# Kernel tuning notes

Measured on AMD Instinct MI355X. Metric: run time of the kernel, lower is better.

Reference implementation:

```python
import jax, jax.numpy as jnp
import numpy as np

L, B, T = 4, 64, 512
H, IN = 1024, 1024


def setup_inputs() -> dict:
    key = jax.random.key(0)
    ks = jax.random.split(key, 6)
    stdv = 1.0 / np.sqrt(H)
    x = jax.random.normal(ks[0], (T, B, IN), dtype=jnp.float32)
    h0 = jax.random.normal(ks[1], (L, B, H), dtype=jnp.float32)
    # stacked per-layer params (input_size == hidden_size so shapes stack)
    w_ih = jax.random.uniform(ks[2], (L, 3 * H, IN), minval=-stdv, maxval=stdv, dtype=jnp.float32)
    w_hh = jax.random.uniform(ks[3], (L, 3 * H, H), minval=-stdv, maxval=stdv, dtype=jnp.float32)
    b_ih = jax.random.uniform(ks[4], (L, 3 * H), minval=-stdv, maxval=stdv, dtype=jnp.float32)
    b_hh = jax.random.uniform(ks[5], (L, 3 * H), minval=-stdv, maxval=stdv, dtype=jnp.float32)
    return {"x": x, "h0": h0, "w_ih": w_ih, "w_hh": w_hh, "b_ih": b_ih, "b_hh": b_hh}


def _gru_forward(x, h0, w_ih, w_hh, b_ih, b_hh):
    hidden = w_hh.shape[-1]

    def layer_fn(inp, layer_args):
        wi, wh, bi, bh, h_prev = layer_args
        gi = inp @ wi.T + bi          # [B, 3H]
        gh = h_prev @ wh.T + bh       # [B, 3H]
        gi_r, gi_z, gi_n = jnp.split(gi, 3, axis=1)
        gh_r, gh_z, gh_n = jnp.split(gh, 3, axis=1)
        r = jax.nn.sigmoid(gi_r + gh_r)
        z = jax.nn.sigmoid(gi_z + gh_z)
        n = jnp.tanh(gi_n + r * gh_n)
        h_new = (1.0 - z) * n + z * h_prev
        return h_new, h_new

    def time_step(h_all, x_t):
        # scan over layers: input flows through, hidden states updated
        _, h_stack = jax.lax.scan(layer_fn, x_t, (w_ih, w_hh, b_ih, b_hh, h_all))
        return h_stack, None

    h_final, _ = jax.lax.scan(time_step, h0, x)
    return h_final  # [L, B, H]


def reference(x, h0, w_ih, w_hh, b_ih, b_hh):
    return _gru_forward(x, h0, w_ih, w_hh, b_ih, b_hh)
```

## Files before the change

### kernel.cpp

```cpp
#include <hip/hip_runtime.h>
#include <hip/hip_bf16.h>

#define NL 4
#define NB 64
#define NT 512
#define NH 1024
#define N3H 3072
#define BH 65536
#define HS_SLOTS 513
#define FSTRIDE 4

typedef __attribute__((ext_vector_type(8))) short short8;
typedef __attribute__((ext_vector_type(4))) float floatx4;

__device__ __forceinline__ short8 ld8(const __hip_bfloat16* p) {
  return *(const short8*)p;
}


__global__ void conv_w_kernel(const float* __restrict__ w_ih,
                              const float* __restrict__ w_hh,
                              __hip_bfloat16* __restrict__ wih_b,
                              __hip_bfloat16* __restrict__ whh_hi,
                              __hip_bfloat16* __restrict__ whh_lo_n) {
  size_t i = (size_t)blockIdx.x * 256 + threadIdx.x;
  if (i >= (size_t)NL * N3H * NH) return;
  wih_b[i] = __float2bfloat16(w_ih[i]);
  float v = w_hh[i];
  __hip_bfloat16 hi = __float2bfloat16(v);
  whh_hi[i] = hi;
  size_t l = i / ((size_t)N3H * NH);
  size_t rem = i - l * ((size_t)N3H * NH);
  size_t row = rem / NH;
  if (row >= (size_t)2 * NH) {
    size_t k = rem - row * NH;
    whh_lo_n[(l * NH + (row - 2 * NH)) * NH + k] =
        __float2bfloat16(v - __bfloat162float(hi));
  }
}

__global__ void conv_x_kernel(const float* __restrict__ x,
                              __hip_bfloat16* __restrict__ xb) {
  size_t i = (size_t)blockIdx.x * 256 + threadIdx.x;
  if (i >= (size_t)NT * NB * NH) return;
  xb[i] = __float2bfloat16(x[i]);
}

__global__ void init_wave_kernel(const float* __restrict__ h0,
                                 float* __restrict__ out,
                                 __hip_bfloat16* __restrict__ hseq,
                                 int* __restrict__ flags) {
  size_t i = (size_t)blockIdx.x * 256 + threadIdx.x;
  if (i < (size_t)5 * 64 * FSTRIDE)
    flags[i] = (i < (size_t)4 * 64 * FSTRIDE) ? 0 : 0x3fffffff;
  if (i >= (size_t)NL * NB * NH) return;
  out[i] = h0[i];
  size_t l = i >> 16;
  size_t j = i & (BH - 1);
  hseq[l * (size_t)HS_SLOTS * BH + j] = __float2bfloat16(h0[i]);
}

__global__ __launch_bounds__(256, 1) void gru_wave_kernel(
    const __hip_bfloat16* __restrict__ whh_hi,
    const __hip_bfloat16* __restrict__ whh_lo,
    const __hip_bfloat16* __restrict__ wih,
    const __hip_bfloat16* __restrict__ xb,
    const float* __restrict__ b_ih,
    const float* __restrict__ b_hh,
    __hip_bfloat16* hseq,
    float* __restrict__ out,
    int* flags) {
  extern __shared__ short lds[];
  const int tid = threadIdx.x;
  const int wv = tid >> 6, lane = tid & 63;
  const int l = blockIdx.x >> 6, g = blockIdx.x & 63;
  const int l15 = lane & 15, quad = lane >> 4;
  const int u = g * 16 + l15;

  const size_t l3h = (size_t)l * N3H;

  {
    const __hip_bfloat16* src;
    if (wv == 0)      src = whh_hi + (l3h + 2 * NH + u) * NH + quad * 8;
    else if (wv == 1) src = whh_lo + (((size_t)l * NH) + u) * NH + quad * 8;
    else if (wv == 2) src = whh_hi + (l3h + u) * NH + quad * 8;
    else              src = whh_hi + (l3h + NH + u) * NH + quad * 8;
    short* dst = lds + wv * 16384 + lane * 8;
#pragma unroll 4
    for (int kc = 0; kc < 32; ++kc)
      *(short8*)(dst + kc * 512) = ld8(src + kc * 32);
  }
  __syncthreads();

  const __hip_bfloat16* vr = wih + (l3h + u) * NH + quad * 8;
  const __hip_bfloat16* vz = wih + (l3h + NH + u) * NH + quad * 8;
  const __hip_bfloat16* vn = wih + (l3h + 2 * NH + u) * NH + quad * 8;
  const float bir = b_ih[l3h + u], biz = b_ih[l3h + NH + u],
              bin = b_ih[l3h + 2 * NH + u];
  const float bhr = b_hh[l3h + u], bhz = b_hh[l3h + NH + u],
              bhn = b_hh[l3h + 2 * NH + u];

  __hip_bfloat16* hs_l = hseq + (size_t)l * HS_SLOTS * BH;
  const __hip_bfloat16* upbase =
      l ? hseq + (size_t)(l - 1) * HS_SLOTS * BH : xb;
  const int upoff = l ? 1 : 0;

  const int row0 = wv * 16 + quad * 4;
  const size_t arow = (size_t)(wv * 16 + l15) * NH + quad * 8;

  float hreg[4];
#pragma unroll
  for (int r = 0; r < 4; ++r)
    hreg[r] = out[(size_t)l * BH + (size_t)(row0 + r) * NH + u];

  const int* fo = flags + (l * 64 + lane) * FSTRIDE;
  const int* fu = flags + ((l ? (l - 1) : 4) * 64 + lane) * FSTRIDE;
  int* fmine = flags + (l * 64 + g) * FSTRIDE;

#pragma unroll 1
  for (int t = 0; t < NT; ++t) {
    while (__hip_atomic_load(fo, __ATOMIC_RELAXED, __HIP_MEMORY_SCOPE_AGENT) < t)
      __builtin_amdgcn_s_sleep(1);
    while (__hip_atomic_load(fu, __ATOMIC_RELAXED, __HIP_MEMORY_SCOPE_AGENT) < t + 1)
      __builtin_amdgcn_s_sleep(1);
    __builtin_amdgcn_sched_barrier(0);
    asm volatile("" ::: "memory");

    const __hip_bfloat16* ob = hs_l + (size_t)t * BH + arow;
    const __hip_bfloat16* ub = upbase + (size_t)(t + upoff) * BH + arow;

    floatx4 z4 = {0.f, 0.f, 0.f, 0.f};
    floatx4 ar = z4, az = z4, anh = z4, anl = z4, gr = z4, gz = z4, gn = z4;

#pragma unroll 4
    for (int kc = 0; kc < 32; ++kc) {
      short8 ho = ld8(ob + kc * 32);
      short8 hu = ld8(ub + kc * 32);
      short8 vrf = ld8(vr + kc * 32);
      short8 vzf = ld8(vz + kc * 32);
      short8 vnf = ld8(vn + kc * 32);
      short8 bnh = *(short8*)(lds + lane * 8 + kc * 512);
      short8 bnl = *(short8*)(lds + 16384 + lane * 8 + kc * 512);
      short8 brf = *(short8*)(lds + 32768 + lane * 8 + kc * 512);
      short8 bzf = *(short8*)(lds + 49152 + lane * 8 + kc * 512);
      ar = __builtin_amdgcn_mfma_f32_16x16x32_bf16(ho, brf, ar, 0, 0, 0);
      az = __builtin_amdgcn_mfma_f32_16x16x32_bf16(ho, bzf, az, 0, 0, 0);
      anh = __builtin_amdgcn_mfma_f32_16x16x32_bf16(ho, bnh, anh, 0, 0, 0);
      anl = __builtin_amdgcn_mfma_f32_16x16x32_bf16(ho, bnl, anl, 0, 0, 0);
      gr = __builtin_amdgcn_mfma_f32_16x16x32_bf16(hu, vrf, gr, 0, 0, 0);
      gz = __builtin_amdgcn_mfma_f32_16x16x32_bf16(hu, vzf, gz, 0, 0, 0);
      gn = __builtin_amdgcn_mfma_f32_16x16x32_bf16(hu, vnf, gn, 0, 0, 0);
    }

    __hip_bfloat16* hw = hs_l + (size_t)(t + 1) * BH;
#pragma unroll
    for (int r = 0; r < 4; ++r) {
      float ghr = ar[r] + bhr;
      float ghz = az[r] + bhz;
      float ghn = anh[r] + anl[r] + bhn;
      float gir = gr[r] + bir;
      float giz = gz[r] + biz;
      float gin = gn[r] + bin;
      float rr = 1.f / (1.f + __expf(-(gir + ghr)));
      float zz = 1.f / (1.f + __expf(-(giz + ghz)));
      float xt = gin + rr * ghn;
      xt = fminf(fmaxf(xt, -15.f), 15.f);
      float e2 = __expf(2.f * xt);
      float nn = (e2 - 1.f) / (e2 + 1.f);
      float hn = (1.f - zz) * nn + zz * hreg[r];
      hreg[r] = hn;
      __hip_bfloat16 hb16 = __float2bfloat16(hn);
      unsigned int v32 = (unsigned int)__builtin_bit_cast(unsigned short, hb16);
      asm volatile("global_store_short %0, %1, off sc0 sc1"
                   :: "v"(hw + (size_t)(row0 + r) * NH + u), "v"(v32)
                   : "memory");
    }
    asm volatile("s_waitcnt vmcnt(0)" ::: "memory");
    __syncthreads();
    if (tid == 0)
      __hip_atomic_store(fmine, t + 1, __ATOMIC_RELAXED, __HIP_MEMORY_SCOPE_AGENT);
  }

#pragma unroll
  for (int r = 0; r < 4; ++r)
    out[(size_t)l * BH + (size_t)(row0 + r) * NH + u] = hreg[r];
}


__global__ void init_out_kernel(const float* __restrict__ h0,
                                float* __restrict__ out,
                                int* __restrict__ flags) {
  size_t i = (size_t)blockIdx.x * 256 + threadIdx.x;
  if (i < (size_t)4 * 64 * FSTRIDE) flags[i] = 0;
  if (i >= (size_t)NL * NB * NH) return;
  out[i] = h0[i];
}

__global__ void init_hbf_kernel(const float* __restrict__ h0_layer,
                                __hip_bfloat16* __restrict__ hb) {
  size_t i = (size_t)blockIdx.x * 256 + threadIdx.x;
  if (i >= (size_t)NB * NH) return;
  hb[i] = __float2bfloat16(h0_layer[i]);
}

__global__ __launch_bounds__(256) void gemm_gi_kernel(
    const __hip_bfloat16* __restrict__ A,
    const __hip_bfloat16* __restrict__ Wb,
    const float* __restrict__ bih,
    float* __restrict__ C) {
  __shared__ short lA[128 * 32];
  __shared__ short lB[128 * 32];
  const int tid = threadIdx.x;
  const int wave = tid >> 6, lane = tid & 63;
  const int l15 = lane & 15, quad = lane >> 4;
  const int m0 = blockIdx.x * 128;
  const int n0 = blockIdx.y * 128;
  const int wm = (wave >> 1) * 64, wn = (wave & 1) * 64;

  const int r1 = tid >> 2, c1 = (tid & 3) * 8;
  const __hip_bfloat16* Arow0 = A + (size_t)(m0 + r1) * NH + c1;
  const __hip_bfloat16* Arow1 = A + (size_t)(m0 + r1 + 64) * NH + c1;
  const __hip_bfloat16* Brow0 = Wb + (size_t)(n0 + r1) * NH + c1;
  const __hip_bfloat16* Brow1 = Wb + (size_t)(n0 + r1 + 64) * NH + c1;

  floatx4 z4 = {0.f, 0.f, 0.f, 0.f};
  floatx4 acc[4][4];
#pragma unroll
  for (int mi = 0; mi < 4; ++mi)
#pragma unroll
    for (int ni = 0; ni < 4; ++ni) acc[mi][ni] = z4;

  for (int kt = 0; kt < 32; ++kt) {
    const int ko = kt * 32;
    short8 a0 = ld8(Arow0 + ko), a1 = ld8(Arow1 + ko);
    short8 b0 = ld8(Brow0 + ko), b1 = ld8(Brow1 + ko);
    __syncthreads();
    *(short8*)(lA + tid * 8) = a0;
    *(short8*)(lA + (tid + 256) * 8) = a1;
    *(short8*)(lB + tid * 8) = b0;
    *(short8*)(lB + (tid + 256) * 8) = b1;
    __syncthreads();
    short8 af[4], bf[4];
#pragma unroll
    for (int mi = 0; mi < 4; ++mi)
      af[mi] = *(short8*)(lA + (wm + mi * 16 + l15) * 32 + quad * 8);
#pragma unroll
    for (int ni = 0; ni < 4; ++ni)
      bf[ni] = *(short8*)(lB + (wn + ni * 16 + l15) * 32 + quad * 8);
#pragma unroll
    for (int mi = 0; mi < 4; ++mi)
#pragma unroll
      for (int ni = 0; ni < 4; ++ni)
        acc[mi][ni] =
            __builtin_amdgcn_mfma_f32_16x16x32_bf16(af[mi], bf[ni], acc[mi][ni], 0, 0, 0);
  }

  const int crow = m0 + wm + quad * 4;
#pragma unroll
  for (int ni = 0; ni < 4; ++ni) {
    const int col = n0 + wn + ni * 16 + l15;
    const float bias = bih[col];
#pragma unroll
    for (int mi = 0; mi < 4; ++mi)
#pragma unroll
      for (int r = 0; r < 4; ++r)
        C[(size_t)(crow + mi * 16 + r) * N3H + col] = acc[mi][ni][r] + bias;
  }
}

__global__ __launch_bounds__(64) void gru_persist_kernel(
    const __hip_bfloat16* __restrict__ whh_hi_l,
    const __hip_bfloat16* __restrict__ whh_lo_l,
    const float* __restrict__ gi_c,
    const float* __restrict__ bhh_l,
    __hip_bfloat16* hbuf,
    __hip_bfloat16* seq_out,
    float* hfp,
    int* flags,
    int s0, int nsteps) {
  const int lane = threadIdx.x;
  const int w = blockIdx.x >> 6;
  const int g = blockIdx.x & 63;
  const int l15 = lane & 15, quad = lane >> 4;
  const int u = g * 16 + l15;

  __shared__ short lds_s[32768];

  {
    const __hip_bfloat16* srch = whh_hi_l + ((size_t)(2 * NH) + u) * NH + quad * 8;
    const __hip_bfloat16* srcl = whh_lo_l + (size_t)u * NH + quad * 8;
    short* dst = lds_s + lane * 8;
#pragma unroll 4
    for (int kc = 0; kc < 32; ++kc) {
      *(short8*)(dst + kc * 512) = ld8(srch + kc * 32);
      *(short8*)(dst + 16384 + kc * 512) = ld8(srcl + kc * 32);
    }
  }
  __syncthreads();

  const int bb = w * 16 + quad * 4;
  float hreg[4];
#pragma unroll
  for (int r = 0; r < 4; ++r) hreg[r] = hfp[(size_t)(bb + r) * NH + u];

  const float bhr = bhh_l[u], bhz = bhh_l[NH + u], bhn = bhh_l[2 * NH + u];
  const __hip_bfloat16* wr = whh_hi_l + (size_t)u * NH + quad * 8;
  const __hip_bfloat16* wz = whh_hi_l + ((size_t)NH + u) * NH + quad * 8;

  int* myflag = flags + (w * 64 + lane) * FSTRIDE;
  int* outflag = flags + (w * 64 + g) * FSTRIDE;
  __hip_bfloat16* hb0 = hbuf;
  __hip_bfloat16* hb1 = hbuf + NB * NH;

  for (int s = s0; s < s0 + nsteps; ++s) {
    const int tc = s - s0;
    const float* gp = gi_c + ((size_t)tc * NB + bb) * N3H + u;
    float gi_r[4], gi_z[4], gi_n[4];
#pragma unroll
    for (int r = 0; r < 4; ++r) {
      gi_r[r] = gp[(size_t)r * N3H];
      gi_z[r] = gp[(size_t)r * N3H + NH];
      gi_n[r] = gp[(size_t)r * N3H + 2 * NH];
    }

    while (__hip_atomic_load(myflag, __ATOMIC_RELAXED, __HIP_MEMORY_SCOPE_AGENT) < s)
      __builtin_amdgcn_s_sleep(1);

    const __hip_bfloat16* hbase =
        ((s & 1) ? hb1 : hb0) + (size_t)(w * 16 + l15) * NH + quad * 8;
    short8 hf[32];
#pragma unroll
    for (int kc = 0; kc < 32; ++kc)
      asm volatile("global_load_dwordx4 %0, %1, off sc0 sc1"
                   : "=v"(hf[kc]) : "v"(hbase + kc * 32));
#pragma unroll
    for (int g8 = 0; g8 < 32; g8 += 8)
      asm volatile("s_waitcnt vmcnt(0)"
                   : "+v"(hf[g8]), "+v"(hf[g8 + 1]), "+v"(hf[g8 + 2]),
                     "+v"(hf[g8 + 3]), "+v"(hf[g8 + 4]), "+v"(hf[g8 + 5]),
                     "+v"(hf[g8 + 6]), "+v"(hf[g8 + 7])
                   :: "memory");

    floatx4 accr = {0.f, 0.f, 0.f, 0.f}, accz = accr, accnh = accr, accnl = accr;
#pragma unroll 8
    for (int kc = 0; kc < 32; ++kc) {
      short8 ah = hf[kc];
      short8 brf = ld8(wr + kc * 32);
      short8 bzf = ld8(wz + kc * 32);
      short8 bnh = *(short8*)(lds_s + lane * 8 + kc * 512);
      short8 bnl = *(short8*)(lds_s + 16384 + lane * 8 + kc * 512);
      accr = __builtin_amdgcn_mfma_f32_16x16x32_bf16(ah, brf, accr, 0, 0, 0);
      accz = __builtin_amdgcn_mfma_f32_16x16x32_bf16(ah, bzf, accz, 0, 0, 0);
      accnh = __builtin_amdgcn_mfma_f32_16x16x32_bf16(ah, bnh, accnh, 0, 0, 0);
      accnl = __builtin_amdgcn_mfma_f32_16x16x32_bf16(ah, bnl, accnl, 0, 0, 0);
    }

    __hip_bfloat16* hout = (s & 1) ? hb0 : hb1;
#pragma unroll
    for (int r = 0; r < 4; ++r) {
      float ghr = accr[r] + bhr;
      float ghz = accz[r] + bhz;
      float ghn = accnh[r] + accnl[r] + bhn;
      float rr = 1.f / (1.f + __expf(-(gi_r[r] + ghr)));
      float zz = 1.f / (1.f + __expf(-(gi_z[r] + ghz)));
      float xt = gi_n[r] + rr * ghn;
      xt = fminf(fmaxf(xt, -15.f), 15.f);
      float e2 = __expf(2.f * xt);
      float nn = (e2 - 1.f) / (e2 + 1.f);
      float hn = (1.f - zz) * nn + zz * hreg[r];
      hreg[r] = hn;
      __hip_bfloat16 hb16 = __float2bfloat16(hn);
      size_t idx = (size_t)(bb + r) * NH + u;
      unsigned int v32 = (unsigned int)__builtin_bit_cast(unsigned short, hb16);
      asm volatile("global_store_short %0, %1, off sc0 sc1"
                   :: "v"(hout + idx), "v"(v32) : "memory");
      if (seq_out) seq_out[(size_t)tc * (NB * NH) + idx] = hb16;
    }
    asm volatile("s_waitcnt vmcnt(0)" ::: "memory");
    if (lane == 0)
      __hip_atomic_store(outflag, s + 1, __ATOMIC_RELAXED, __HIP_MEMORY_SCOPE_AGENT);
  }

#pragma unroll
  for (int r = 0; r < 4; ++r) hfp[(size_t)(bb + r) * NH + u] = hreg[r];
}

extern "C" void kernel_launch(void* const* d_in, const int* in_sizes, int n_in,
                              void* d_out, int out_size, void* d_ws, size_t ws_size,
                              hipStream_t stream) {
  const float* x = (const float*)d_in[0];
  const float* h0 = (const float*)d_in[1];
  const float* w_ih = (const float*)d_in[2];
  const float* w_hh = (const float*)d_in[3];
  const float* b_ih = (const float*)d_in[4];
  const float* b_hh = (const float*)d_in[5];
  float* out = (float*)d_out;
  (void)in_sizes; (void)n_in; (void)out_size;

  char* ws = (char*)d_ws;
  const size_t wsz = (size_t)NL * N3H * NH * 2;
  const size_t lsz = (size_t)NL * NH * NH * 2;
  const size_t xsz = (size_t)NT * NB * NH * 2;
  const size_t hssz = (size_t)NL * HS_SLOTS * BH * 2;
  const size_t fsz = (size_t)5 * 64 * FSTRIDE * 4;
  const size_t need_wave = wsz * 2 + lsz + xsz + hssz + fsz + 1024;

  if (ws_size >= need_wave) {
    size_t off = 0;
    __hip_bfloat16* wih_b = (__hip_bfloat16*)(ws + off); off += wsz;
    __hip_bfloat16* whh_hi = (__hip_bfloat16*)(ws + off); off += wsz;
    __hip_bfloat16* whh_lo = (__hip_bfloat16*)(ws + off); off += lsz;
    __hip_bfloat16* xb = (__hip_bfloat16*)(ws + off); off += xsz;
    __hip_bfloat16* hseq = (__hip_bfloat16*)(ws + off); off += hssz;
    int* flags = (int*)(ws + off); off += fsz;

    static bool attr_set = false;
    if (!attr_set) {
      (void)hipFuncSetAttribute((const void*)gru_wave_kernel,
                                hipFuncAttributeMaxDynamicSharedMemorySize,
                                131072);
      attr_set = true;
    }

    {
      size_t n = (size_t)NL * N3H * NH;
      conv_w_kernel<<<dim3((n + 255) / 256), dim3(256), 0, stream>>>(
          w_ih, w_hh, wih_b, whh_hi, whh_lo);
    }
    {
      size_t n = (size_t)NT * NB * NH;
      conv_x_kernel<<<dim3((n + 255) / 256), dim3(256), 0, stream>>>(x, xb);
    }
    {
      size_t n = (size_t)NL * NB * NH;
      init_wave_kernel<<<dim3((n + 255) / 256), dim3(256), 0, stream>>>(
          h0, out, hseq, flags);
    }
    gru_wave_kernel<<<dim3(256), dim3(256), 131072, stream>>>(
        whh_hi, whh_lo, wih_b, xb, b_ih, b_hh, hseq, out, flags);
    return;
  }

  size_t off = 0;
  const size_t ssz = (size_t)NT * NB * NH * 2;
  __hip_bfloat16* wih_b = (__hip_bfloat16*)(ws + off); off += wsz;
  __hip_bfloat16* whh_hi = (__hip_bfloat16*)(ws + off); off += wsz;
  __hip_bfloat16* whh_lo = (__hip_bfloat16*)(ws + off); off += lsz;
  __hip_bfloat16* seqA = (__hip_bfloat16*)(ws + off); off += ssz;
  __hip_bfloat16* seqB = (__hip_bfloat16*)(ws + off); off += ssz;
  __hip_bfloat16* hbuf = (__hip_bfloat16*)(ws + off); off += (size_t)2 * NB * NH * 2;
  int* flags = (int*)(ws + off); off += (size_t)4 * 64 * FSTRIDE * 4;
  off = (off + 255) & ~(size_t)255;
  float* gi_buf = (float*)(ws + off);

  long long avail = (long long)ws_size - (long long)off;
  int TC = 256;
  while (TC > 2 && (long long)TC * NB * N3H * 4 > avail) TC >>= 1;

  {
    size_t n = (size_t)NL * N3H * NH;
    conv_w_kernel<<<dim3((n + 255) / 256), dim3(256), 0, stream>>>(
        w_ih, w_hh, wih_b, whh_hi, whh_lo);
  }
  {
    size_t n = (size_t)NT * NB * NH;
    conv_x_kernel<<<dim3((n + 255) / 256), dim3(256), 0, stream>>>(x, seqA);
  }
  {
    size_t n = (size_t)NL * NB * NH;
    init_out_kernel<<<dim3((n + 255) / 256), dim3(256), 0, stream>>>(h0, out, flags);
  }

  const size_t bh = (size_t)NB * NH;
  const int nchunks = NT / TC;
  for (int l = 0; l < NL; ++l) {
    init_hbf_kernel<<<dim3((bh + 255) / 256), dim3(256), 0, stream>>>(
        h0 + (size_t)l * bh, hbuf);
    const __hip_bfloat16* cur = (l & 1) ? seqB : seqA;
    __hip_bfloat16* nxt = (l == NL - 1) ? (__hip_bfloat16*)nullptr
                                        : ((l & 1) ? seqA : seqB);
    const __hip_bfloat16* wih_l = wih_b + (size_t)l * N3H * NH;
    const __hip_bfloat16* whha_l = whh_hi + (size_t)l * N3H * NH;
    const __hip_bfloat16* whhb_l = whh_lo + (size_t)l * NH * NH;
    const float* bih_l = b_ih + (size_t)l * N3H;
    const float* bhh_l = b_hh + (size_t)l * N3H;
    float* hfp_l = out + (size_t)l * bh;
    for (int c = 0; c < nchunks; ++c) {
      const __hip_bfloat16* Ac = cur + (size_t)c * TC * bh;
      gemm_gi_kernel<<<dim3(TC * NB / 128, N3H / 128), dim3(256), 0, stream>>>(
          Ac, wih_l, bih_l, gi_buf);
      __hip_bfloat16* so = nxt ? nxt + (size_t)c * TC * bh : (__hip_bfloat16*)nullptr;
      gru_persist_kernel<<<dim3(256), dim3(64), 0, stream>>>(
          whha_l, whhb_l, gi_buf, bhh_l, hbuf, so, hfp_l, flags,
          l * NT + c * TC, TC);
    }
  }
}
```

Baseline: 13.11 ms.

## Stage W_in n-gate weights in LDS and prefetch hidden rows into registers

The n-gate input weights are now loaded once into a fifth LDS slab, raising dynamic shared memory to 160KB, so they are no longer streamed from global memory every timestep. The loads of the own-layer and upstream hidden states for all 32 k-chunks are hoisted into register arrays ahead of a fully unrolled MFMA loop, so the loads can be issued together and latency overlapped. The two flag spin-waits are merged into one loop. The larger register arrays raise register pressure and risk spilling, and the larger LDS footprint relies on the MI355X shared memory capacity.

```diff
diff --git a/kernel.cpp b/kernel.cpp
--- a/kernel.cpp
+++ b/kernel.cpp
@@ -89,12 +89,18 @@
 #pragma unroll 4
     for (int kc = 0; kc < 32; ++kc)
       *(short8*)(dst + kc * 512) = ld8(src + kc * 32);
+    const __hip_bfloat16* srcn = wih + (l3h + 2 * NH + u) * NH + quad * 8;
+    short* dstn = lds + 4 * 16384 + lane * 8;
+#pragma unroll
+    for (int kk = 0; kk < 8; ++kk) {
+      int kc = wv * 8 + kk;
+      *(short8*)(dstn + kc * 512) = ld8(srcn + kc * 32);
+    }
   }
   __syncthreads();
 
   const __hip_bfloat16* vr = wih + (l3h + u) * NH + quad * 8;
   const __hip_bfloat16* vz = wih + (l3h + NH + u) * NH + quad * 8;
-  const __hip_bfloat16* vn = wih + (l3h + 2 * NH + u) * NH + quad * 8;
   const float bir = b_ih[l3h + u], biz = b_ih[l3h + NH + u],
               bin = b_ih[l3h + 2 * NH + u];
   const float bhr = b_hh[l3h + u], bhz = b_hh[l3h + NH + u],
@@ -119,9 +125,8 @@
 
 #pragma unroll 1
   for (int t = 0; t < NT; ++t) {
-    while (__hip_atomic_load(fo, __ATOMIC_RELAXED, __HIP_MEMORY_SCOPE_AGENT) < t)
-      __builtin_amdgcn_s_sleep(1);
-    while (__hip_atomic_load(fu, __ATOMIC_RELAXED, __HIP_MEMORY_SCOPE_AGENT) < t + 1)
+    while (__hip_atomic_load(fo, __ATOMIC_RELAXED, __HIP_MEMORY_SCOPE_AGENT) < t ||
+           __hip_atomic_load(fu, __ATOMIC_RELAXED, __HIP_MEMORY_SCOPE_AGENT) < t + 1)
       __builtin_amdgcn_s_sleep(1);
     __builtin_amdgcn_sched_barrier(0);
     asm volatile("" ::: "memory");
@@ -129,27 +134,31 @@
     const __hip_bfloat16* ob = hs_l + (size_t)t * BH + arow;
     const __hip_bfloat16* ub = upbase + (size_t)(t + upoff) * BH + arow;
 
+    short8 ho[32], hu[32];
+#pragma unroll
+    for (int kc = 0; kc < 32; ++kc) ho[kc] = ld8(ob + kc * 32);
+#pragma unroll
+    for (int kc = 0; kc < 32; ++kc) hu[kc] = ld8(ub + kc * 32);
+
     floatx4 z4 = {0.f, 0.f, 0.f, 0.f};
     floatx4 ar = z4, az = z4, anh = z4, anl = z4, gr = z4, gz = z4, gn = z4;
 
-#pragma unroll 4
+#pragma unroll
     for (int kc = 0; kc < 32; ++kc) {
-      short8 ho = ld8(ob + kc * 32);
-      short8 hu = ld8(ub + kc * 32);
       short8 vrf = ld8(vr + kc * 32);
       short8 vzf = ld8(vz + kc * 32);
-      short8 vnf = ld8(vn + kc * 32);
       short8 bnh = *(short8*)(lds + lane * 8 + kc * 512);
       short8 bnl = *(short8*)(lds + 16384 + lane * 8 + kc * 512);
       short8 brf = *(short8*)(lds + 32768 + lane * 8 + kc * 512);
       short8 bzf = *(short8*)(lds + 49152 + lane * 8 + kc * 512);
-      ar = __builtin_amdgcn_mfma_f32_16x16x32_bf16(ho, brf, ar, 0, 0, 0);
-      az = __builtin_amdgcn_mfma_f32_16x16x32_bf16(ho, bzf, az, 0, 0, 0);
-      anh = __builtin_amdgcn_mfma_f32_16x16x32_bf16(ho, bnh, anh, 0, 0, 0);
-      anl = __builtin_amdgcn_mfma_f32_16x16x32_bf16(ho, bnl, anl, 0, 0, 0);
-      gr = __builtin_amdgcn_mfma_f32_16x16x32_bf16(hu, vrf, gr, 0, 0, 0);
-      gz = __builtin_amdgcn_mfma_f32_16x16x32_bf16(hu, vzf, gz, 0, 0, 0);
-      gn = __builtin_amdgcn_mfma_f32_16x16x32_bf16(hu, vnf, gn, 0, 0, 0);
+      short8 vnf = *(short8*)(lds + 65536 + lane * 8 + kc * 512);
+      ar = __builtin_amdgcn_mfma_f32_16x16x32_bf16(ho[kc], brf, ar, 0, 0, 0);
+      az = __builtin_amdgcn_mfma_f32_16x16x32_bf16(ho[kc], bzf, az, 0, 0, 0);
+      anh = __builtin_amdgcn_mfma_f32_16x16x32_bf16(ho[kc], bnh, anh, 0, 0, 0);
+      anl = __builtin_amdgcn_mfma_f32_16x16x32_bf16(ho[kc], bnl, anl, 0, 0, 0);
+      gr = __builtin_amdgcn_mfma_f32_16x16x32_bf16(hu[kc], vrf, gr, 0, 0, 0);
+      gz = __builtin_amdgcn_mfma_f32_16x16x32_bf16(hu[kc], vzf, gz, 0, 0, 0);
+      gn = __builtin_amdgcn_mfma_f32_16x16x32_bf16(hu[kc], vnf, gn, 0, 0, 0);
     }
 
     __hip_bfloat16* hw = hs_l + (size_t)(t + 1) * BH;
@@ -418,7 +427,7 @@
     if (!attr_set) {
       (void)hipFuncSetAttribute((const void*)gru_wave_kernel,
                                 hipFuncAttributeMaxDynamicSharedMemorySize,
-                                131072);
+                                163840);
       attr_set = true;
     }
 
@@ -436,7 +445,7 @@
       init_wave_kernel<<<dim3((n + 255) / 256), dim3(256), 0, stream>>>(
           h0, out, hseq, flags);
     }
-    gru_wave_kernel<<<dim3(256), dim3(256), 131072, stream>>>(
+    gru_wave_kernel<<<dim3(256), dim3(256), 163840, stream>>>(
         whh_hi, whh_lo, wih_b, xb, b_ih, b_hh, hseq, out, flags);
     return;
   }
```

Result: faster. 10.56 ms (-19.5%).
